# Performance work log

Hardware: AMD Instinct MI355X
Metric: run time of the kernel (lower is better)

Reference implementation:

```python
import jax, jax.numpy as jnp
import numpy as np

D_MODEL = 1024
D_FF = 4096
N_EXPERTS = 8
TOP_K = 2
BATCH, SEQ = 4, 1024


def setup_inputs() -> dict:
    key = jax.random.key(0)
    ks = jax.random.split(key, 5)
    x = jax.random.normal(ks[0], (BATCH, SEQ, D_MODEL), jnp.float32)
    Wr = jax.random.normal(ks[1], (D_MODEL, N_EXPERTS), jnp.float32) * (D_MODEL ** -0.5)
    W1 = jax.random.normal(ks[2], (N_EXPERTS, D_MODEL, D_FF), jnp.float32) * (D_MODEL ** -0.5)
    b1 = jnp.zeros((N_EXPERTS, D_FF), jnp.float32)
    W2 = jax.random.normal(ks[3], (N_EXPERTS, D_FF, D_MODEL), jnp.float32) * (D_FF ** -0.5)
    b2 = jnp.zeros((N_EXPERTS, D_MODEL), jnp.float32)
    return {"x": x, "Wr": Wr, "W1": W1, "b1": b1, "W2": W2, "b2": b2}


def reference(x, Wr, W1, b1, W2, b2):
    B, S, D = x.shape
    E = Wr.shape[1]
    xf = x.reshape(-1, D)                         # [T, D], T = B*S
    # Router: softmax over experts, pick top-k, renormalize gates over the k picks
    probs = jax.nn.softmax(xf @ Wr, axis=-1)      # [T, E]
    top_v, top_i = jax.lax.top_k(probs, TOP_K)    # [T, K]
    gates = top_v / jnp.sum(top_v, axis=-1, keepdims=True)
    # Combine weights per (token, expert): weight is gate if expert selected else 0
    cw = jnp.sum(gates[:, :, None] * jax.nn.one_hot(top_i, E, dtype=x.dtype), axis=1)  # [T, E]
    # Expert MLPs: loop over the small fixed expert count, weighted scatter-add combine
    out = jnp.zeros_like(xf)
    for e in range(E):
        h = jax.nn.relu(xf @ W1[e] + b1[e])       # [T, d_ff]
        y = h @ W2[e] + b2[e]                     # [T, D]
        out = out + cw[:, e:e + 1] * y
    return out.reshape(x.shape)
```

## Files before the change

### kernel.cpp

```cpp
#include <hip/hip_runtime.h>


#define T_TOK 4096
#define DMODEL 1024
#define DFF 4096
#define NE 8
#define CAP 9216
#define MT_CAP (CAP / 128)

typedef __bf16 bf16x8 __attribute__((ext_vector_type(8)));
typedef float f32x4 __attribute__((ext_vector_type(4)));

__device__ __forceinline__ unsigned short f2bf(float f) {
    union { float f; unsigned u; } v; v.f = f;
    unsigned r = v.u + 0x7fffu + ((v.u >> 16) & 1u);
    return (unsigned short)(r >> 16);
}

__device__ __forceinline__ void gld16(const unsigned short* g, unsigned short* l) {
    __builtin_amdgcn_global_load_lds(
        (const __attribute__((address_space(1))) unsigned int*)g,
        (__attribute__((address_space(3))) unsigned int*)l, 16, 0, 0);
}

__global__ __launch_bounds__(256) void k_router(const float* __restrict__ x,
                                                const float* __restrict__ Wr,
                                                int* __restrict__ meta,
                                                int* __restrict__ tg_idx,
                                                float* __restrict__ tg_gate) {
    int wave = threadIdx.x >> 6, lane = threadIdx.x & 63;
    int t = blockIdx.x * 4 + wave;
    double acc[NE];
#pragma unroll
    for (int e = 0; e < NE; e++) acc[e] = 0.0;
    const float* xr = x + (size_t)t * DMODEL;
#pragma unroll 4
    for (int j = 0; j < 16; j++) {
        int k = j * 64 + lane;
        double xv = (double)xr[k];
        const float4* wr = (const float4*)(Wr + k * NE);
        float4 w0 = wr[0], w1 = wr[1];
        acc[0] += xv * (double)w0.x; acc[1] += xv * (double)w0.y;
        acc[2] += xv * (double)w0.z; acc[3] += xv * (double)w0.w;
        acc[4] += xv * (double)w1.x; acc[5] += xv * (double)w1.y;
        acc[6] += xv * (double)w1.z; acc[7] += xv * (double)w1.w;
    }
#pragma unroll
    for (int off = 32; off; off >>= 1)
#pragma unroll
        for (int e = 0; e < NE; e++) acc[e] += __shfl_xor(acc[e], off);
    if (lane == 0) {
        double v1 = -1e300, v2 = -1e300; int i1 = 0, i2 = 0;
#pragma unroll
        for (int e = 0; e < NE; e++) {
            double v = acc[e];
            if (v > v1) { v2 = v1; i2 = i1; v1 = v; i1 = e; }
            else if (v > v2) { v2 = v; i2 = e; }
        }
        double g1 = 1.0 / (1.0 + exp(v2 - v1));
        tg_idx[t * 2] = i1; tg_idx[t * 2 + 1] = i2;
        tg_gate[t * 2] = (float)g1; tg_gate[t * 2 + 1] = (float)(1.0 - g1);
        atomicAdd(&meta[i1], 1);
        atomicAdd(&meta[i2], 1);
    }
}

__global__ void k_scan(int* __restrict__ meta) {
    if (threadIdx.x == 0) {
        int acc = 0;
        for (int e = 0; e < NE; e++) {
            int a = (meta[e] + 127) & ~127;
            meta[16 + e] = a;
            meta[24 + e] = acc;
            acc += a;
        }
        meta[24 + NE] = acc;
        meta[33] = acc;
    }
}

__global__ __launch_bounds__(256) void k_build(const int* __restrict__ tg_idx,
                                               const float* __restrict__ tg_gate,
                                               int* __restrict__ meta,
                                               int* __restrict__ tos,
                                               float* __restrict__ gos,
                                               int* __restrict__ sot) {
    int t = blockIdx.x * 256 + threadIdx.x;
#pragma unroll
    for (int kk = 0; kk < 2; kk++) {
        int e = tg_idx[t * 2 + kk];
        int pos = atomicAdd(&meta[8 + e], 1);
        int slot = meta[24 + e] + pos;
        tos[slot] = t;
        gos[slot] = tg_gate[t * 2 + kk];
        sot[t * 2 + kk] = slot;
    }
}

__global__ __launch_bounds__(256) void k_gather(const float* __restrict__ x,
                                                const int* __restrict__ tos,
                                                const int* __restrict__ meta,
                                                unsigned short* __restrict__ xg) {
    int s = blockIdx.x;
    if (s >= meta[33]) return;
    int t = tos[s];
    int tid = threadIdx.x;
#pragma unroll
    for (int j = 0; j < 4; j++) {
        int k = tid + j * 256;
        float v = (t >= 0) ? x[(size_t)t * DMODEL + k] : 0.f;
        xg[(size_t)s * DMODEL + k] = f2bf(v);
    }
}

__global__ __launch_bounds__(256) void k_transpose(const float* __restrict__ in,
                                                   unsigned short* __restrict__ out,
                                                   int R, int C) {
    int e = blockIdx.z;
    const float* src = in + (size_t)e * R * C;
    unsigned short* dst = out + (size_t)e * R * C;
    int g = threadIdx.x >> 3, l8 = threadIdx.x & 7;
    int rb = blockIdx.y * 64 + l8 * 8;
    int cb = blockIdx.x * 128 + g * 4;
    f32x4 v[8];
#pragma unroll
    for (int i = 0; i < 8; i++)
        v[i] = *(const f32x4*)&src[(size_t)(rb + i) * C + cb];
#pragma unroll
    for (int j = 0; j < 4; j++) {
        unsigned short o[8];
#pragma unroll
        for (int i = 0; i < 8; i++) o[i] = f2bf(v[i][j]);
        *(uint4*)&dst[(size_t)(cb + j) * R + rb] = *(uint4*)o;
    }
}

template <int MODE>
__global__ __launch_bounds__(256, 4) void k_gemm(const unsigned short* __restrict__ A,
                                                 const unsigned short* __restrict__ Bt,
                                                 const float* __restrict__ bias,
                                                 const int* __restrict__ meta,
                                                 unsigned short* __restrict__ H,
                                                 float* __restrict__ Y) {
    constexpr int KFULL = (MODE == 1) ? DMODEL : DFF;
    constexpr int K     = (MODE == 1) ? DMODEL : DFF / 2;
    constexpr int N     = (MODE == 1) ? DFF : DMODEL;

    int L = blockIdx.x;
    int xcd = L & 7, c = L >> 3;
    int sgrp = c / MT_CAP, mt = c - sgrp * MT_CAP;
    int s = (sgrp << 3) | xcd;
    int e, kq, nt;
    if constexpr (MODE == 1) { e = s >> 5; nt = s & 31; kq = 0; }
    else                     { e = s >> 4; kq = (s >> 3) & 1; nt = s & 7; }
    if (mt * 128 >= meta[16 + e]) return;
    int row0 = meta[24 + e] + mt * 128;
    int col0 = nt * 128;
    const unsigned short* Ae = A + (size_t)row0 * KFULL + kq * K;
    const unsigned short* Be = Bt + (size_t)e * N * KFULL + (size_t)col0 * KFULL + kq * K;
    const float* be = bias + (size_t)e * N;

    __shared__ __align__(16) unsigned short As[128 * 64];
    __shared__ __align__(16) unsigned short Bs[128 * 64];

    int tid = threadIdx.x;
    int lane = tid & 63, wave = tid >> 6;
    int wy = wave >> 1, wx = wave & 1;
    int q = lane >> 4, r16 = lane & 15;

    int srow = lane >> 3;
    int schunk = (lane & 7) ^ srow;
    int sgoff = srow * KFULL + schunk * 8;

    f32x4 acc[4][4];
#pragma unroll
    for (int i = 0; i < 4; i++)
#pragma unroll
        for (int j = 0; j < 4; j++) acc[i][j] = (f32x4){0.f, 0.f, 0.f, 0.f};

    for (int k0 = 0; k0 < K; k0 += 64) {
        __syncthreads();
#pragma unroll
        for (int it = 0; it < 4; it++) {
            int gr = wave * 32 + it * 8;
            gld16(Ae + (size_t)gr * KFULL + k0 + sgoff, &As[gr * 64]);
            gld16(Be + (size_t)gr * KFULL + k0 + sgoff, &Bs[gr * 64]);
        }
        __syncthreads();
#pragma unroll
        for (int ks = 0; ks < 2; ks++) {
            bf16x8 af[4], bfr[4];
            int sw = (r16 & 7);
#pragma unroll
            for (int i = 0; i < 4; i++) {
                int m = wy * 64 + i * 16 + r16;
                af[i] = *(const bf16x8*)&As[m * 64 + (((ks * 4 + q) ^ sw) << 3)];
            }
#pragma unroll
            for (int j = 0; j < 4; j++) {
                int n = wx * 64 + j * 16 + r16;
                bfr[j] = *(const bf16x8*)&Bs[n * 64 + (((ks * 4 + q) ^ sw) << 3)];
            }
#pragma unroll
            for (int i = 0; i < 4; i++)
#pragma unroll
                for (int j = 0; j < 4; j++)
                    acc[i][j] = __builtin_amdgcn_mfma_f32_16x16x32_bf16(af[i], bfr[j], acc[i][j], 0, 0, 0);
        }
    }

    if constexpr (MODE == 1) {
#pragma unroll
        for (int i = 0; i < 4; i++) {
#pragma unroll
            for (int rr = 0; rr < 4; rr++) {
                int gs = row0 + wy * 64 + i * 16 + q * 4 + rr;
#pragma unroll
                for (int j = 0; j < 4; j++) {
                    int gn = col0 + wx * 64 + j * 16 + r16;
                    float v = acc[i][j][rr] + be[gn];
                    H[(size_t)gs * DFF + gn] = f2bf(v > 0.f ? v : 0.f);
                }
            }
        }
    } else {
        float* Yp = Y + (size_t)kq * CAP * DMODEL;
#pragma unroll
        for (int i = 0; i < 4; i++) {
#pragma unroll
            for (int rr = 0; rr < 4; rr++) {
                int gs = row0 + wy * 64 + i * 16 + q * 4 + rr;
#pragma unroll
                for (int j = 0; j < 4; j++) {
                    int gn = col0 + wx * 64 + j * 16 + r16;
                    Yp[(size_t)gs * DMODEL + gn] = acc[i][j][rr];
                }
            }
        }
    }
}

__global__ __launch_bounds__(256) void k_combine(const float* __restrict__ Y,
                                                 const int* __restrict__ tg_idx,
                                                 const float* __restrict__ tg_gate,
                                                 const int* __restrict__ sot,
                                                 const float* __restrict__ b2,
                                                 float* __restrict__ out) {
    int t = blockIdx.x;
    int e0 = tg_idx[t * 2], e1 = tg_idx[t * 2 + 1];
    float g0 = tg_gate[t * 2], g1 = tg_gate[t * 2 + 1];
    int s0 = sot[t * 2], s1 = sot[t * 2 + 1];
    const float* y0 = Y;
    const float* y1 = Y + (size_t)CAP * DMODEL;
    int d = threadIdx.x * 4;
    f32x4 a0 = *(const f32x4*)&y0[(size_t)s0 * DMODEL + d];
    f32x4 b0 = *(const f32x4*)&y1[(size_t)s0 * DMODEL + d];
    f32x4 a1 = *(const f32x4*)&y0[(size_t)s1 * DMODEL + d];
    f32x4 b1v = *(const f32x4*)&y1[(size_t)s1 * DMODEL + d];
    f32x4 c0 = *(const f32x4*)&b2[(size_t)e0 * DMODEL + d];
    f32x4 c1 = *(const f32x4*)&b2[(size_t)e1 * DMODEL + d];
    f32x4 r;
#pragma unroll
    for (int i = 0; i < 4; i++)
        r[i] = g0 * (a0[i] + b0[i] + c0[i]) + g1 * (a1[i] + b1v[i] + c1[i]);
    *(f32x4*)&out[(size_t)t * DMODEL + d] = r;
}

extern "C" void kernel_launch(void* const* d_in, const int* in_sizes, int n_in,
                              void* d_out, int out_size, void* d_ws, size_t ws_size,
                              hipStream_t stream) {
    const float* x  = (const float*)d_in[0];
    const float* Wr = (const float*)d_in[1];
    const float* W1 = (const float*)d_in[2];
    const float* b1 = (const float*)d_in[3];
    const float* W2 = (const float*)d_in[4];
    const float* b2 = (const float*)d_in[5];
    float* out = (float*)d_out;

    char* p = (char*)d_ws;
    auto alloc = [&](size_t bytes) {
        char* q = p;
        p += (bytes + 255) & ~(size_t)255;
        return q;
    };
    int*   meta    = (int*)alloc(64 * 4);
    int*   tg_idx  = (int*)alloc((size_t)T_TOK * 2 * 4);
    float* tg_gate = (float*)alloc((size_t)T_TOK * 2 * 4);
    int*   tos     = (int*)alloc((size_t)CAP * 4);
    float* gos     = (float*)alloc((size_t)CAP * 4);
    int*   sot     = (int*)alloc((size_t)T_TOK * 2 * 4);
    unsigned short* xg  = (unsigned short*)alloc((size_t)CAP * DMODEL * 2);
    unsigned short* W1t = (unsigned short*)alloc((size_t)NE * DMODEL * DFF * 2);
    unsigned short* W2t = (unsigned short*)alloc((size_t)NE * DMODEL * DFF * 2);
    unsigned short* h   = (unsigned short*)alloc((size_t)CAP * DFF * 2);
    float* y = (float*)xg;

    hipMemsetAsync(meta, 0, 64 * 4, stream);
    hipMemsetAsync(tos, 0xFF, (size_t)CAP * 4, stream);

    k_router<<<T_TOK / 4, 256, 0, stream>>>(x, Wr, meta, tg_idx, tg_gate);
    k_scan<<<1, 64, 0, stream>>>(meta);
    k_build<<<T_TOK / 256, 256, 0, stream>>>(tg_idx, tg_gate, meta, tos, gos, sot);
    k_gather<<<CAP, 256, 0, stream>>>(x, tos, meta, xg);
    k_transpose<<<dim3(DFF / 128, DMODEL / 64, NE), 256, 0, stream>>>(W1, W1t, DMODEL, DFF);
    k_gemm<1><<<dim3(NE * (DFF / 128) * MT_CAP), 256, 0, stream>>>(xg, W1t, b1, meta, h, nullptr);
    k_transpose<<<dim3(DMODEL / 128, DFF / 64, NE), 256, 0, stream>>>(W2, W2t, DFF, DMODEL);
    k_gemm<2><<<dim3(NE * 2 * (DMODEL / 128) * MT_CAP), 256, 0, stream>>>(h, W2t, b2, meta, nullptr, y);
    k_combine<<<T_TOK, 256, 0, stream>>>(y, tg_idx, tg_gate, sot, b2, out);
}
```

Measured before the change: 692.7 us.

## Pipeline expert GEMMs with multi-stage LDS prefetch and 256-row tiles

```diff
diff --git a/kernel.cpp b/kernel.cpp
--- a/kernel.cpp
+++ b/kernel.cpp
@@ -5,8 +5,8 @@
 #define DMODEL 1024
 #define DFF 4096
 #define NE 8
-#define CAP 9216
-#define MT_CAP (CAP / 128)
+#define CAP 10240
+#define MT_CAP 32
 
 typedef __bf16 bf16x8 __attribute__((ext_vector_type(8)));
 typedef float f32x4 __attribute__((ext_vector_type(4)));
@@ -69,7 +69,7 @@
     if (threadIdx.x == 0) {
         int acc = 0;
         for (int e = 0; e < NE; e++) {
-            int a = (meta[e] + 127) & ~127;
+            int a = (meta[e] + 255) & ~255;
             meta[16 + e] = a;
             meta[24 + e] = acc;
             acc += a;
@@ -136,7 +136,7 @@
 }
 
 template <int MODE>
-__global__ __launch_bounds__(256, 4) void k_gemm(const unsigned short* __restrict__ A,
+__global__ __launch_bounds__(512, 2) void k_gemm(const unsigned short* __restrict__ A,
                                                  const unsigned short* __restrict__ Bt,
                                                  const float* __restrict__ bias,
                                                  const int* __restrict__ meta,
@@ -145,32 +145,39 @@
     constexpr int KFULL = (MODE == 1) ? DMODEL : DFF;
     constexpr int K     = (MODE == 1) ? DMODEL : DFF / 2;
     constexpr int N     = (MODE == 1) ? DFF : DMODEL;
+    constexpr int NPH   = K / 32;
 
     int L = blockIdx.x;
     int xcd = L & 7, c = L >> 3;
-    int sgrp = c / MT_CAP, mt = c - sgrp * MT_CAP;
+    int sgrp = c >> 5, mt = c & 31;
     int s = (sgrp << 3) | xcd;
     int e, kq, nt;
     if constexpr (MODE == 1) { e = s >> 5; nt = s & 31; kq = 0; }
     else                     { e = s >> 4; kq = (s >> 3) & 1; nt = s & 7; }
-    if (mt * 128 >= meta[16 + e]) return;
-    int row0 = meta[24 + e] + mt * 128;
+    if (mt * 256 >= meta[16 + e]) return;
+    int row0 = meta[24 + e] + mt * 256;
     int col0 = nt * 128;
     const unsigned short* Ae = A + (size_t)row0 * KFULL + kq * K;
     const unsigned short* Be = Bt + (size_t)e * N * KFULL + (size_t)col0 * KFULL + kq * K;
     const float* be = bias + (size_t)e * N;
 
-    __shared__ __align__(16) unsigned short As[128 * 64];
-    __shared__ __align__(16) unsigned short Bs[128 * 64];
+    __shared__ __align__(16) unsigned short As[2][2][256 * 32];
+    __shared__ __align__(16) unsigned short Bs[2][2][128 * 32];
 
     int tid = threadIdx.x;
-    int lane = tid & 63, wave = tid >> 6;
-    int wy = wave >> 1, wx = wave & 1;
+    int lane = tid & 63, wv = tid >> 6;
+    int wm = wv >> 1, wn = wv & 1;
     int q = lane >> 4, r16 = lane & 15;
-
-    int srow = lane >> 3;
-    int schunk = (lane & 7) ^ srow;
-    int sgoff = srow * KFULL + schunk * 8;
+    int srow = lane >> 2, scol = lane & 3;
+
+    auto stage = [&](int u) {
+        int p = (u >> 1) & 1, kh = u & 1;
+        const unsigned short* ga = Ae + (size_t)(wv * 32 + srow) * KFULL + u * 32 + scol * 8;
+        gld16(ga,                      &As[p][kh][(wv * 32) * 32]);
+        gld16(ga + (size_t)16 * KFULL, &As[p][kh][(wv * 32 + 16) * 32]);
+        const unsigned short* gb = Be + (size_t)(wv * 16 + srow) * KFULL + u * 32 + scol * 8;
+        gld16(gb,                      &Bs[p][kh][(wv * 16) * 32]);
+    };
 
     f32x4 acc[4][4];
 #pragma unroll
@@ -178,35 +185,41 @@
 #pragma unroll
         for (int j = 0; j < 4; j++) acc[i][j] = (f32x4){0.f, 0.f, 0.f, 0.f};
 
-    for (int k0 = 0; k0 < K; k0 += 64) {
-        __syncthreads();
-#pragma unroll
-        for (int it = 0; it < 4; it++) {
-            int gr = wave * 32 + it * 8;
-            gld16(Ae + (size_t)gr * KFULL + k0 + sgoff, &As[gr * 64]);
-            gld16(Be + (size_t)gr * KFULL + k0 + sgoff, &Bs[gr * 64]);
-        }
-        __syncthreads();
-#pragma unroll
-        for (int ks = 0; ks < 2; ks++) {
-            bf16x8 af[4], bfr[4];
-            int sw = (r16 & 7);
-#pragma unroll
-            for (int i = 0; i < 4; i++) {
-                int m = wy * 64 + i * 16 + r16;
-                af[i] = *(const bf16x8*)&As[m * 64 + (((ks * 4 + q) ^ sw) << 3)];
-            }
-#pragma unroll
-            for (int j = 0; j < 4; j++) {
-                int n = wx * 64 + j * 16 + r16;
-                bfr[j] = *(const bf16x8*)&Bs[n * 64 + (((ks * 4 + q) ^ sw) << 3)];
-            }
-#pragma unroll
-            for (int i = 0; i < 4; i++)
-#pragma unroll
-                for (int j = 0; j < 4; j++)
-                    acc[i][j] = __builtin_amdgcn_mfma_f32_16x16x32_bf16(af[i], bfr[j], acc[i][j], 0, 0, 0);
-        }
+    stage(0); stage(1); stage(2);
+    asm volatile("s_waitcnt vmcnt(6)" ::: "memory");
+    __builtin_amdgcn_s_barrier();
+
+#pragma unroll 4
+    for (int ph = 0; ph < NPH; ph++) {
+        int p = (ph >> 1) & 1, kh = ph & 1;
+        const unsigned short* Ar = &As[p][kh][0];
+        const unsigned short* Br = &Bs[p][kh][0];
+        bf16x8 af[4], bfr[4];
+#pragma unroll
+        for (int i = 0; i < 4; i++)
+            af[i] = *(const bf16x8*)&Ar[(wm * 64 + i * 16 + r16) * 32 + q * 8];
+#pragma unroll
+        for (int j = 0; j < 4; j++)
+            bfr[j] = *(const bf16x8*)&Br[(wn * 64 + j * 16 + r16) * 32 + q * 8];
+
+        if (ph + 3 < NPH) stage(ph + 3);
+
+        if (ph < NPH - 3)       asm volatile("s_waitcnt vmcnt(6)" ::: "memory");
+        else if (ph == NPH - 3) asm volatile("s_waitcnt vmcnt(3)" ::: "memory");
+        else                    asm volatile("s_waitcnt vmcnt(0)" ::: "memory");
+        __builtin_amdgcn_s_barrier();
+
+        asm volatile("s_waitcnt lgkmcnt(0)" ::: "memory");
+        __builtin_amdgcn_sched_barrier(0);
+        __builtin_amdgcn_s_setprio(1);
+#pragma unroll
+        for (int i = 0; i < 4; i++)
+#pragma unroll
+            for (int j = 0; j < 4; j++)
+                acc[i][j] = __builtin_amdgcn_mfma_f32_16x16x32_bf16(af[i], bfr[j], acc[i][j], 0, 0, 0);
+        __builtin_amdgcn_s_setprio(0);
+        __builtin_amdgcn_sched_barrier(0);
+        __builtin_amdgcn_s_barrier();
     }
 
     if constexpr (MODE == 1) {
@@ -214,10 +227,10 @@
         for (int i = 0; i < 4; i++) {
 #pragma unroll
             for (int rr = 0; rr < 4; rr++) {
-                int gs = row0 + wy * 64 + i * 16 + q * 4 + rr;
+                int gs = row0 + wm * 64 + i * 16 + q * 4 + rr;
 #pragma unroll
                 for (int j = 0; j < 4; j++) {
-                    int gn = col0 + wx * 64 + j * 16 + r16;
+                    int gn = col0 + wn * 64 + j * 16 + r16;
                     float v = acc[i][j][rr] + be[gn];
                     H[(size_t)gs * DFF + gn] = f2bf(v > 0.f ? v : 0.f);
                 }
@@ -229,10 +242,10 @@
         for (int i = 0; i < 4; i++) {
 #pragma unroll
             for (int rr = 0; rr < 4; rr++) {
-                int gs = row0 + wy * 64 + i * 16 + q * 4 + rr;
+                int gs = row0 + wm * 64 + i * 16 + q * 4 + rr;
 #pragma unroll
                 for (int j = 0; j < 4; j++) {
-                    int gn = col0 + wx * 64 + j * 16 + r16;
+                    int gn = col0 + wn * 64 + j * 16 + r16;
                     Yp[(size_t)gs * DMODEL + gn] = acc[i][j][rr];
                 }
             }
@@ -303,8 +316,8 @@
     k_build<<<T_TOK / 256, 256, 0, stream>>>(tg_idx, tg_gate, meta, tos, gos, sot);
     k_gather<<<CAP, 256, 0, stream>>>(x, tos, meta, xg);
     k_transpose<<<dim3(DFF / 128, DMODEL / 64, NE), 256, 0, stream>>>(W1, W1t, DMODEL, DFF);
-    k_gemm<1><<<dim3(NE * (DFF / 128) * MT_CAP), 256, 0, stream>>>(xg, W1t, b1, meta, h, nullptr);
+    k_gemm<1><<<dim3(NE * 32 * MT_CAP), 512, 0, stream>>>(xg, W1t, b1, meta, h, nullptr);
     k_transpose<<<dim3(DMODEL / 128, DFF / 64, NE), 256, 0, stream>>>(W2, W2t, DFF, DMODEL);
-    k_gemm<2><<<dim3(NE * 2 * (DMODEL / 128) * MT_CAP), 256, 0, stream>>>(h, W2t, b2, meta, nullptr, y);
+    k_gemm<2><<<dim3(NE * 2 * 8 * MT_CAP), 512, 0, stream>>>(h, W2t, b2, meta, nullptr, y);
     k_combine<<<T_TOK, 256, 0, stream>>>(y, tg_idx, tg_gate, sot, b2, out);
 }
```

Result: slower. 781.7 us (+12.8%).
